# Kernel tuning notes

Measured on AMD Instinct MI355X. Metric: run time of the kernel, lower is better.

The kernel has to match this reference:

```python
import jax, jax.numpy as jnp
import numpy as np

N_SETS, N_POINTS, D_FEAT = 8, 4096, 16
K = 16


def setup_inputs() -> dict:
    key = jax.random.key(0)
    x = jax.random.normal(key, (N_SETS, N_POINTS, D_FEAT), dtype=jnp.float32)
    return {"x": x, "k": K}


def reference(x, k):
    """Faithful kNN-graph construction.

    x: (N, M, D) point sets. Returns (src, dst) flattened edge lists with
    per-sample node-ID offsets (node j of set i -> global id i*M + j), plus
    the top-k squared distances (the selection values).
    """
    n_samples, n_points, _ = x.shape
    # pairwise squared distance: ||xi||^2 + ||xj||^2 - 2 xi.xj  -> (N, M, M)
    x2s = jnp.sum(x * x, axis=-1, keepdims=True)
    dist = x2s + jnp.swapaxes(x2s, -1, -2) - 2.0 * jnp.einsum("nmd,npd->nmp", x, x)
    # k smallest distances per row (argtopk descending=False)
    neg_vals, k_indices = jax.lax.top_k(-dist, k)            # (N, M, k)
    topk_dist = -neg_vals
    per_sample_offset = (jnp.arange(n_samples, dtype=jnp.int32) * n_points)[:, None, None]
    dst = k_indices.astype(jnp.int32) + per_sample_offset     # neighbor ids
    src = jnp.broadcast_to(
        jnp.arange(n_points, dtype=jnp.int32)[None, :, None], k_indices.shape
    ) + per_sample_offset                                     # query ids
    return src.reshape(-1), dst.reshape(-1), topk_dist
```

## Files before the change

kernel.cpp:

```cpp
#include <hip/hip_runtime.h>
#include <hip/hip_bf16.h>

#define NSETS 8
#define NPTS  4096
#define DF    16
#define KNN   16
#define QPB   64
#define NCH   8
#define BLK   (QPB * NCH)
#define TILE  512
#define NTILE (NPTS / TILE)
#define SLICE (TILE / NCH)
#define NEDGE (NSETS * NPTS * KNN)

#define RES      8
#define FLUSH_AT 5
#define GRP      4

#define FEAT_B   (TILE * DF * 4)
#define NRM_B    (TILE * 4)
#define RESV_OFF (FEAT_B + NRM_B)
#define SMEM_B   (RESV_OFF + RES * BLK * 8)

__global__ __launch_bounds__(BLK) void knn_kernel(const float* __restrict__ x,
                                                  float* __restrict__ out) {
    __shared__ float tau_sh[QPB];
    __shared__ __align__(16) char smem[SMEM_B];
    float4* feat4 = (float4*)smem;
    float*  nrm_t = (float*)(smem + FEAT_B);
    float2* resv  = (float2*)(smem + RESV_OFF);
    float*          lds_d = (float*)smem;
    unsigned short* lds_i = (unsigned short*)(smem + BLK * KNN * 4);

    const int t    = threadIdx.x;
    const int lane = t & 63;
    const int wv   = t >> 6;
    const int set  = blockIdx.x >> 6;
    const int q0   = (blockIdx.x & 63) * QPB;
    const int q    = q0 + lane;

    const float* xs = x + (size_t)set * NPTS * DF;

    if (t < QPB) tau_sh[t] = 3.0e38f;

    float qn[DF];
    float q2;
    {
        const float4* qp = (const float4*)(xs + (size_t)q * DF);
        float4 a = qp[0], b = qp[1], g = qp[2], d = qp[3];
        float r0 = __fadd_rn(__fmul_rn(a.x, a.x), __fmul_rn(g.x, g.x));
        float r1 = __fadd_rn(__fmul_rn(a.y, a.y), __fmul_rn(g.y, g.y));
        float r2 = __fadd_rn(__fmul_rn(a.z, a.z), __fmul_rn(g.z, g.z));
        float r3 = __fadd_rn(__fmul_rn(a.w, a.w), __fmul_rn(g.w, g.w));
        float r4 = __fadd_rn(__fmul_rn(b.x, b.x), __fmul_rn(d.x, d.x));
        float r5 = __fadd_rn(__fmul_rn(b.y, b.y), __fmul_rn(d.y, d.y));
        float r6 = __fadd_rn(__fmul_rn(b.z, b.z), __fmul_rn(d.z, d.z));
        float r7 = __fadd_rn(__fmul_rn(b.w, b.w), __fmul_rn(d.w, d.w));
        q2 = __fadd_rn(__fadd_rn(__fadd_rn(r0, r1), __fadd_rn(r2, r3)),
                       __fadd_rn(__fadd_rn(r4, r5), __fadd_rn(r6, r7)));
        qn[0]=a.x; qn[1]=a.y; qn[2]=a.z; qn[3]=a.w;
        qn[4]=b.x; qn[5]=b.y; qn[6]=b.z; qn[7]=b.w;
        qn[8]=g.x; qn[9]=g.y; qn[10]=g.z; qn[11]=g.w;
        qn[12]=d.x; qn[13]=d.y; qn[14]=d.z; qn[15]=d.w;
#pragma unroll
        for (int d2 = 0; d2 < DF; ++d2) qn[d2] = -2.0f * qn[d2];
    }

    float Ld[KNN];
    int   Li[KNN];
#pragma unroll
    for (int j = 0; j < KNN; ++j) { Ld[j] = 3.0e38f; Li[j] = 0; }
    int cnt = 0;

    auto flush = [&]() {
        for (int e = 0; e < RES; ++e) {
            if (!__any(e < cnt)) break;
            float2 en = resv[e * BLK + t];
            const float d  = (e < cnt) ? en.x : 3.0e38f;
            const int   ci = __float_as_int(en.y);
            if (d < Ld[KNN - 1]) {
#pragma unroll
                for (int j = KNN - 1; j >= 1; --j) {
                    const bool sh   = d < Ld[j - 1];
                    const bool here = d < Ld[j];
                    const float nd = sh ? Ld[j - 1] : (here ? d  : Ld[j]);
                    const int   ni = sh ? Li[j - 1] : (here ? ci : Li[j]);
                    Ld[j] = nd; Li[j] = ni;
                }
                if (d < Ld[0]) { Ld[0] = d; Li[0] = ci; }
            }
        }
        cnt = 0;
        volatile float* ts = (volatile float*)tau_sh;
        float cur = ts[lane];
        ts[lane] = fminf(cur, Ld[KNN - 1]);
    };

    for (int tile = 0; tile < NTILE; ++tile) {
        __syncthreads();
        {
            const int c = tile * TILE + t;
            const float4* p = (const float4*)(xs + (size_t)c * DF);
            float4 a = p[0], b = p[1], g = p[2], d = p[3];
            float r0 = __fadd_rn(__fmul_rn(a.x, a.x), __fmul_rn(g.x, g.x));
            float r1 = __fadd_rn(__fmul_rn(a.y, a.y), __fmul_rn(g.y, g.y));
            float r2 = __fadd_rn(__fmul_rn(a.z, a.z), __fmul_rn(g.z, g.z));
            float r3 = __fadd_rn(__fmul_rn(a.w, a.w), __fmul_rn(g.w, g.w));
            float r4 = __fadd_rn(__fmul_rn(b.x, b.x), __fmul_rn(d.x, d.x));
            float r5 = __fadd_rn(__fmul_rn(b.y, b.y), __fmul_rn(d.y, d.y));
            float r6 = __fadd_rn(__fmul_rn(b.z, b.z), __fmul_rn(d.z, d.z));
            float r7 = __fadd_rn(__fmul_rn(b.w, b.w), __fmul_rn(d.w, d.w));
            feat4[0 * TILE + t] = a;
            feat4[1 * TILE + t] = b;
            feat4[2 * TILE + t] = g;
            feat4[3 * TILE + t] = d;
            nrm_t[t] = __fadd_rn(
                __fadd_rn(__fadd_rn(r0, r1), __fadd_rn(r2, r3)),
                __fadd_rn(__fadd_rn(r4, r5), __fadd_rn(r6, r7)));
        }
        __syncthreads();

        const int lbase = wv * SLICE;
        const int gbase = tile * TILE + lbase;

        for (int g = 0; g < SLICE; g += GRP) {
            const float tsh = ((volatile float*)tau_sh)[lane];
            const float tau = fminf(tsh, Ld[KNN - 1]);
#pragma unroll
            for (int u = 0; u < GRP; ++u) {
                const int lc = lbase + g + u;
                float4 f0 = feat4[0 * TILE + lc];
                float4 f1 = feat4[1 * TILE + lc];
                float4 f2 = feat4[2 * TILE + lc];
                float4 f3 = feat4[3 * TILE + lc];
                const float nc = nrm_t[lc];
                float dot = 0.f;
                dot = fmaf(qn[0],  f0.x, dot); dot = fmaf(qn[1],  f0.y, dot);
                dot = fmaf(qn[2],  f0.z, dot); dot = fmaf(qn[3],  f0.w, dot);
                dot = fmaf(qn[4],  f1.x, dot); dot = fmaf(qn[5],  f1.y, dot);
                dot = fmaf(qn[6],  f1.z, dot); dot = fmaf(qn[7],  f1.w, dot);
                dot = fmaf(qn[8],  f2.x, dot); dot = fmaf(qn[9],  f2.y, dot);
                dot = fmaf(qn[10], f2.z, dot); dot = fmaf(qn[11], f2.w, dot);
                dot = fmaf(qn[12], f3.x, dot); dot = fmaf(qn[13], f3.y, dot);
                dot = fmaf(qn[14], f3.z, dot); dot = fmaf(qn[15], f3.w, dot);
                const float dist = __fadd_rn(__fadd_rn(q2, nc), dot);
                if (dist <= tau) {
                    resv[cnt * BLK + t] =
                        make_float2(dist, __int_as_float(gbase + g + u));
                    ++cnt;
                }
            }
            if (__any(cnt >= FLUSH_AT)) flush();
        }
    }
    flush();

    __syncthreads();
#pragma unroll
    for (int j = 0; j < KNN; ++j) {
        lds_d[t * KNN + j] = Ld[j];
        lds_i[t * KNN + j] = (unsigned short)Li[j];
    }
    __syncthreads();

    if (t < QPB) {
        const int l = t;
        float h[NCH];
        int   hi[NCH];
        int   p[NCH];
#pragma unroll
        for (int w2 = 0; w2 < NCH; ++w2) {
            p[w2]  = 0;
            h[w2]  = lds_d[(w2 * QPB + l) * KNN];
            hi[w2] = (int)lds_i[(w2 * QPB + l) * KNN];
        }

        const int    gq = set * NPTS + q0 + l;
        const size_t eb = (size_t)gq * KNN;
        float* osrc = out;
        float* odst = out + (size_t)NEDGE;
        float* odis = out + 2 * (size_t)NEDGE;
        const float srcf = (float)gq;

        for (int e = 0; e < KNN; ++e) {
            float best = h[0];
            int   bi   = hi[0];
            int   bw   = 0;
#pragma unroll
            for (int w2 = 1; w2 < NCH; ++w2) {
                const bool better = (h[w2] < best) ||
                                    (h[w2] == best && hi[w2] < bi);
                if (better) { best = h[w2]; bi = hi[w2]; bw = w2; }
            }

#pragma unroll
            for (int w2 = 0; w2 < NCH; ++w2) {
                if (bw == w2) {
                    ++p[w2];
                    if (p[w2] < KNN) {
                        h[w2]  = lds_d[(w2 * QPB + l) * KNN + p[w2]];
                        hi[w2] = (int)lds_i[(w2 * QPB + l) * KNN + p[w2]];
                    } else {
                        h[w2]  = 3.0e38f;
                        hi[w2] = 0x7FFFFFFF;
                    }
                }
            }

            osrc[eb + e] = srcf;
            odst[eb + e] = (float)(set * NPTS + bi);
            odis[eb + e] = best;
        }
    }
}

extern "C" void kernel_launch(void* const* d_in, const int* in_sizes, int n_in,
                              void* d_out, int out_size, void* d_ws, size_t ws_size,
                              hipStream_t stream) {
    (void)in_sizes; (void)n_in; (void)out_size; (void)d_ws; (void)ws_size;
    const float* x = (const float*)d_in[0];
    float* out = (float*)d_out;

    knn_kernel<<<NSETS * (NPTS / QPB), BLK, 0, stream>>>(x, out);
}
```

Baseline: 228.8 us.

## Replace insertion-sort flush with bitonic merge networks on packed 64-bit keys

Candidates are packed into 64-bit keys made of an order-preserving flipped float distance and the index. Each flush then sorts the reservoir with a fixed 19-compare network and merges it into the sorted top-16 list with a bitonic min-then-clean step. This removes the per-candidate serial insertion loops and their divergent early exit. The LDS staging stride is also padded to 17 to reduce bank conflicts, and the threshold is now kept in a register. In exchange, every flush runs the full network on 64-bit compares even when few candidates are present.

```diff
diff --git a/kernel.cpp b/kernel.cpp
--- a/kernel.cpp
+++ b/kernel.cpp
@@ -1,5 +1,6 @@
 #include <hip/hip_runtime.h>
-#include <hip/hip_bf16.h>
+
+typedef unsigned long long u64;
 
 #define NSETS 8
 #define NPTS  4096
@@ -21,6 +22,21 @@
 #define NRM_B    (TILE * 4)
 #define RESV_OFF (FEAT_B + NRM_B)
 #define SMEM_B   (RESV_OFF + RES * BLK * 8)
+#define MPAD     17
+
+__device__ __forceinline__ unsigned flip_f(float d) {
+    unsigned b = __float_as_uint(d);
+    return (b & 0x80000000u) ? ~b : (b | 0x80000000u);
+}
+__device__ __forceinline__ float unflip_f(unsigned u) {
+    unsigned b = (u & 0x80000000u) ? (u ^ 0x80000000u) : ~u;
+    return __uint_as_float(b);
+}
+
+#define CEB(i, j) { u64 _a = B[i], _b = B[j]; bool _c = _b < _a; \
+                    B[i] = _c ? _b : _a; B[j] = _c ? _a : _b; }
+#define CEL(i, j) { u64 _a = Lk[i], _b = Lk[j]; bool _c = _b < _a; \
+                    Lk[i] = _c ? _b : _a; Lk[j] = _c ? _a : _b; }
 
 __global__ __launch_bounds__(BLK) void knn_kernel(const float* __restrict__ x,
                                                   float* __restrict__ out) {
@@ -28,9 +44,9 @@
     __shared__ __align__(16) char smem[SMEM_B];
     float4* feat4 = (float4*)smem;
     float*  nrm_t = (float*)(smem + FEAT_B);
-    float2* resv  = (float2*)(smem + RESV_OFF);
+    u64*    resv  = (u64*)(smem + RESV_OFF);
     float*          lds_d = (float*)smem;
-    unsigned short* lds_i = (unsigned short*)(smem + BLK * KNN * 4);
+    unsigned short* lds_i = (unsigned short*)(smem + BLK * MPAD * 4);
 
     const int t    = threadIdx.x;
     const int lane = t & 63;
@@ -66,34 +82,45 @@
         for (int d2 = 0; d2 < DF; ++d2) qn[d2] = -2.0f * qn[d2];
     }
 
-    float Ld[KNN];
-    int   Li[KNN];
-#pragma unroll
-    for (int j = 0; j < KNN; ++j) { Ld[j] = 3.0e38f; Li[j] = 0; }
-    int cnt = 0;
+    const u64 SENT = ((u64)flip_f(3.0e38f) << 32) | 0xFFFFFFFFull;
+    u64   Lk[KNN];
+#pragma unroll
+    for (int j = 0; j < KNN; ++j) Lk[j] = SENT;
+    float tau_reg = 3.0e38f;
+    int   cnt = 0;
 
     auto flush = [&]() {
+        u64 B[RES];
+#pragma unroll
         for (int e = 0; e < RES; ++e) {
-            if (!__any(e < cnt)) break;
-            float2 en = resv[e * BLK + t];
-            const float d  = (e < cnt) ? en.x : 3.0e38f;
-            const int   ci = __float_as_int(en.y);
-            if (d < Ld[KNN - 1]) {
-#pragma unroll
-                for (int j = KNN - 1; j >= 1; --j) {
-                    const bool sh   = d < Ld[j - 1];
-                    const bool here = d < Ld[j];
-                    const float nd = sh ? Ld[j - 1] : (here ? d  : Ld[j]);
-                    const int   ni = sh ? Li[j - 1] : (here ? ci : Li[j]);
-                    Ld[j] = nd; Li[j] = ni;
-                }
-                if (d < Ld[0]) { Ld[0] = d; Li[0] = ci; }
-            }
-        }
+            u64 v = resv[e * BLK + t];
+            B[e] = (e < cnt) ? v : SENT;
+        }
+        CEB(0,1) CEB(2,3) CEB(4,5) CEB(6,7)
+        CEB(0,2) CEB(1,3) CEB(4,6) CEB(5,7)
+        CEB(1,2) CEB(5,6)
+        CEB(0,4) CEB(1,5) CEB(2,6) CEB(3,7)
+        CEB(2,4) CEB(3,5)
+        CEB(1,2) CEB(3,4) CEB(5,6)
+#pragma unroll
+        for (int i = 0; i < RES; ++i) {
+            u64 a = Lk[KNN - 1 - i], b = B[i];
+            Lk[KNN - 1 - i] = (b < a) ? b : a;
+        }
+        CEL(0,8)  CEL(1,9)  CEL(2,10) CEL(3,11)
+        CEL(4,12) CEL(5,13) CEL(6,14) CEL(7,15)
+        CEL(0,4)  CEL(1,5)  CEL(2,6)  CEL(3,7)
+        CEL(8,12) CEL(9,13) CEL(10,14) CEL(11,15)
+        CEL(0,2)  CEL(1,3)  CEL(4,6)  CEL(5,7)
+        CEL(8,10) CEL(9,11) CEL(12,14) CEL(13,15)
+        CEL(0,1)  CEL(2,3)  CEL(4,5)  CEL(6,7)
+        CEL(8,9)  CEL(10,11) CEL(12,13) CEL(14,15)
         cnt = 0;
+        const float kth = unflip_f((unsigned)(Lk[KNN - 1] >> 32));
+        tau_reg = kth;
         volatile float* ts = (volatile float*)tau_sh;
         float cur = ts[lane];
-        ts[lane] = fminf(cur, Ld[KNN - 1]);
+        ts[lane] = fminf(cur, kth);
     };
 
     for (int tile = 0; tile < NTILE; ++tile) {
@@ -125,7 +152,7 @@
 
         for (int g = 0; g < SLICE; g += GRP) {
             const float tsh = ((volatile float*)tau_sh)[lane];
-            const float tau = fminf(tsh, Ld[KNN - 1]);
+            const float tau = fminf(tsh, tau_reg);
 #pragma unroll
             for (int u = 0; u < GRP; ++u) {
                 const int lc = lbase + g + u;
@@ -146,7 +173,7 @@
                 const float dist = __fadd_rn(__fadd_rn(q2, nc), dot);
                 if (dist <= tau) {
                     resv[cnt * BLK + t] =
-                        make_float2(dist, __int_as_float(gbase + g + u));
+                        ((u64)flip_f(dist) << 32) | (unsigned)(gbase + g + u);
                     ++cnt;
                 }
             }
@@ -158,8 +185,8 @@
     __syncthreads();
 #pragma unroll
     for (int j = 0; j < KNN; ++j) {
-        lds_d[t * KNN + j] = Ld[j];
-        lds_i[t * KNN + j] = (unsigned short)Li[j];
+        lds_d[t * MPAD + j] = unflip_f((unsigned)(Lk[j] >> 32));
+        lds_i[t * MPAD + j] = (unsigned short)(Lk[j] & 0xFFFFu);
     }
     __syncthreads();
 
@@ -171,8 +198,8 @@
 #pragma unroll
         for (int w2 = 0; w2 < NCH; ++w2) {
             p[w2]  = 0;
-            h[w2]  = lds_d[(w2 * QPB + l) * KNN];
-            hi[w2] = (int)lds_i[(w2 * QPB + l) * KNN];
+            h[w2]  = lds_d[(w2 * QPB + l) * MPAD];
+            hi[w2] = (int)lds_i[(w2 * QPB + l) * MPAD];
         }
 
         const int    gq = set * NPTS + q0 + l;
@@ -198,8 +225,8 @@
                 if (bw == w2) {
                     ++p[w2];
                     if (p[w2] < KNN) {
-                        h[w2]  = lds_d[(w2 * QPB + l) * KNN + p[w2]];
-                        hi[w2] = (int)lds_i[(w2 * QPB + l) * KNN + p[w2]];
+                        h[w2]  = lds_d[(w2 * QPB + l) * MPAD + p[w2]];
+                        hi[w2] = (int)lds_i[(w2 * QPB + l) * MPAD + p[w2]];
                     } else {
                         h[w2]  = 3.0e38f;
                         hi[w2] = 0x7FFFFFFF;
```

Result: no change. 232.3 us (+1.6%).
